# Optimization experiments

Hardware: AMD Instinct MI355X
Metric: run time of the kernel (lower is better)

## Reference

```python
import jax, jax.numpy as jnp
import numpy as np

D_MODEL = 256
N_HEAD = 8
HEAD_DIM = D_MODEL // N_HEAD
N_TOTAL = 24576
B, T = 64, 512


def setup_inputs() -> dict:
    key = jax.random.key(0)
    ks = jax.random.split(key, 12)
    s = 1.0 / np.sqrt(D_MODEL)
    return {
        "x": jax.random.normal(ks[0], (N_TOTAL, D_MODEL), jnp.float32),
        "Wq": jax.random.uniform(ks[1], (D_MODEL, D_MODEL), jnp.float32, -s, s),
        "bq": jax.random.uniform(ks[2], (D_MODEL,), jnp.float32, -s, s),
        "Wk": jax.random.uniform(ks[3], (D_MODEL, D_MODEL), jnp.float32, -s, s),
        "bk": jax.random.uniform(ks[4], (D_MODEL,), jnp.float32, -s, s),
        "Wv": jax.random.uniform(ks[5], (D_MODEL, D_MODEL), jnp.float32, -s, s),
        "bv": jax.random.uniform(ks[6], (D_MODEL,), jnp.float32, -s, s),
        "Wp": jax.random.uniform(ks[7], (D_MODEL, D_MODEL), jnp.float32, -s, s),
        "bp": jax.random.uniform(ks[8], (D_MODEL,), jnp.float32, -s, s),
        "padpack_index": jax.random.randint(ks[9], (B, T), 0, N_TOTAL, jnp.int64 if jax.config.jax_enable_x64 else jnp.int32),
        "padpack_batch": jax.random.randint(ks[10], (B, T), 0, B, jnp.int32),
        "padpack_inverse_index": jax.random.randint(ks[11], (N_TOTAL,), 0, B * T, jnp.int64 if jax.config.jax_enable_x64 else jnp.int32),
    }


def reference(x, Wq, bq, Wk, bk, Wv, bv, Wp, bp, padpack_index, padpack_batch, padpack_inverse_index):
    # gather ragged tokens into packed [B, T, C]
    xp = x[padpack_index]
    # mask: True where packed slots share the same segment id (matches
    # original masked_fill(batch_i == batch_j, -1e9))
    mask = padpack_batch[:, :, None] == padpack_batch[:, None, :]  # [B,T,T]
    # QKV projections (torch Linear: x @ W.T + b), split heads
    def heads(w, b):
        h = xp @ w.T + b
        return h.reshape(B, T, N_HEAD, HEAD_DIM).transpose(0, 2, 1, 3)  # [B,H,T,D]
    q, k, v = heads(Wq, bq), heads(Wk, bk), heads(Wv, bv)
    att = jnp.einsum("bhtd,bhsd->bhts", q, k) * (1.0 / np.sqrt(HEAD_DIM))
    att = jnp.where(mask[:, None], jnp.float32(-1e9), att)
    att = jax.nn.softmax(att, axis=-1)
    y = jnp.einsum("bhts,bhsd->bhtd", att, v)  # [B,H,T,D]
    y = y.transpose(0, 2, 1, 3).reshape(B, T, D_MODEL)
    y = y @ Wp.T + bp
    # scatter back to ragged layout
    return y.reshape(B * T, D_MODEL)[padpack_inverse_index]
```

## Files before the change

### kernel.cpp

```cpp
#include <hip/hip_runtime.h>


typedef __attribute__((ext_vector_type(8))) short short8;
typedef __attribute__((ext_vector_type(4))) float f32x4;

#define N_TOTAL 24576
#define B_ 64
#define T_ 512
#define M_TOK 32768
#define DM 256
#define NH 8
#define HD 32

#define QSCALE 0.25503463f

__device__ __forceinline__ unsigned short f2bf(float f) {
  unsigned int u = __float_as_uint(f);
  u += 0x7fffu + ((u >> 16) & 1u);
  return (unsigned short)(u >> 16);
}

__device__ __forceinline__ void gl_lds16(const void* g, void* l) {
  __builtin_amdgcn_global_load_lds(
      (const __attribute__((address_space(1))) unsigned int*)g,
      (__attribute__((address_space(3))) unsigned int*)l, 16, 0, 0);
}

__global__ __launch_bounds__(256) void pack_kernel(
    const float* __restrict__ x, const float* __restrict__ Wq,
    const float* __restrict__ Wk, const float* __restrict__ Wv,
    const float* __restrict__ Wp, const float* __restrict__ bq,
    const float* __restrict__ bk, const float* __restrict__ bv,
    const int* __restrict__ idx,
    short* __restrict__ XP, short* __restrict__ WCAT, short* __restrict__ WPb,
    float* __restrict__ BCAT) {
  int gid = blockIdx.x * 256 + threadIdx.x;
  if (gid < 768)
    BCAT[gid] = (gid < 256) ? bq[gid] : (gid < 512 ? bk[gid - 256] : bv[gid - 512]);
  const float* src;
  short* dst;
  if (gid < 1048576) {
    int row = gid >> 5, seg = gid & 31;
    src = x + (size_t)idx[row] * DM + seg * 8;
    dst = XP + (size_t)gid * 8;
  } else if (gid < 1073152) {
    int u = gid - 1048576;
    int f = u >> 5, seg = u & 31;
    const float* W = (f < 256) ? Wq : ((f < 512) ? Wk : Wv);
    src = W + (size_t)(f & 255) * DM + seg * 8;
    dst = WCAT + (size_t)u * 8;
  } else {
    int u = gid - 1073152;
    src = Wp + (size_t)u * 8;
    dst = WPb + (size_t)u * 8;
  }
  const float4* s4 = (const float4*)src;
  float4 a = s4[0], b = s4[1];
  short8 o;
  o[0] = (short)f2bf(a.x); o[1] = (short)f2bf(a.y);
  o[2] = (short)f2bf(a.z); o[3] = (short)f2bf(a.w);
  o[4] = (short)f2bf(b.x); o[5] = (short)f2bf(b.y);
  o[6] = (short)f2bf(b.z); o[7] = (short)f2bf(b.w);
  *(short8*)dst = o;
}

__global__ __launch_bounds__(256) void qkv_gemm(
    const short* __restrict__ XP, const short* __restrict__ WCAT,
    const float* __restrict__ BCAT,
    unsigned short* __restrict__ Qb, unsigned short* __restrict__ Kb,
    unsigned short* __restrict__ Vt) {
  __shared__ __align__(16) char smem[3 * 16384];
  int tid = threadIdx.x;
  int lane = tid & 63, w = tid >> 6;
  int i = lane & 15, q = lane >> 4;
  int m0 = blockIdx.x * 128, n0 = blockIdx.y * 128;
  int wm = (w & 1) * 64, wn = (w >> 1) * 64;
  int csa = q ^ ((i >> 1) & 3);

  f32x4 zf = {0.f, 0.f, 0.f, 0.f};
  f32x4 acc[4][4];
#pragma unroll
  for (int mt = 0; mt < 4; mt++)
#pragma unroll
    for (int nt = 0; nt < 4; nt++) acc[mt][nt] = zf;

  auto stage = [&](int k, int s) {
#pragma unroll
    for (int p = 0; p < 2; p++) {
      int U = p * 256 + tid;
      int row = U >> 2, c = U & 3;
      int cs = c ^ ((row >> 1) & 3);
      gl_lds16(XP + (size_t)(m0 + row) * DM + k * 32 + cs * 8,
               smem + s * 16384 + U * 16);
      gl_lds16(WCAT + (size_t)(n0 + row) * DM + k * 32 + cs * 8,
               smem + s * 16384 + 8192 + U * 16);
    }
  };

  stage(0, 0);
  stage(1, 1);
#pragma unroll
  for (int k = 0; k < 8; k++) {
    if (k == 7)
      asm volatile("s_waitcnt vmcnt(0) lgkmcnt(0)\ns_barrier" ::: "memory");
    else
      asm volatile("s_waitcnt vmcnt(4) lgkmcnt(0)\ns_barrier" ::: "memory");
    const short* Asb = (const short*)(smem + (k % 3) * 16384);
    const short* Bsb = Asb + 8192 / 2;
    short8 a[4], bfr[4];
#pragma unroll
    for (int mt = 0; mt < 4; mt++)
      a[mt] = *(const short8*)&Asb[(wm + mt * 16 + i) * 32 + csa * 8];
#pragma unroll
    for (int nt = 0; nt < 4; nt++)
      bfr[nt] = *(const short8*)&Bsb[(wn + nt * 16 + i) * 32 + csa * 8];
    if (k < 6) stage(k + 2, (k + 2) % 3);
#pragma unroll
    for (int mt = 0; mt < 4; mt++)
#pragma unroll
      for (int nt = 0; nt < 4; nt++)
        acc[mt][nt] = __builtin_amdgcn_mfma_f32_16x16x32_bf16(a[mt], bfr[nt], acc[mt][nt], 0, 0, 0);
  }

#pragma unroll
  for (int nt = 0; nt < 4; nt++) {
    int f = n0 + wn + nt * 16 + i;
    float bias = BCAT[f];
    int which = f >> 8;
    int fw = f & 255;
    int hh = fw >> 5, dd = fw & 31;
#pragma unroll
    for (int mt = 0; mt < 4; mt++) {
#pragma unroll
      for (int r = 0; r < 4; r++) {
        int token = m0 + wm + mt * 16 + q * 4 + r;
        int bb = token >> 9, tt = token & 511;
        int bh = bb * NH + hh;
        float val = acc[mt][nt][r] + bias;
        if (which == 0)
          Qb[((size_t)bh * T_ + tt) * HD + dd] = f2bf(val * QSCALE);
        else if (which == 1)
          Kb[((size_t)bh * T_ + tt) * HD + dd] = f2bf(val);
        else
          Vt[((size_t)bh * HD + dd) * T_ + tt] = f2bf(val);
      }
    }
  }
}

__global__ __launch_bounds__(256) void attn_kernel(
    const short* __restrict__ Qb, const short* __restrict__ Kb,
    const short* __restrict__ Vt, const int* __restrict__ batch,
    unsigned short* __restrict__ Y) {
  __shared__ __align__(16) short pscr[4][64 * 40];
  __shared__ int sbat[T_];
  int tid = threadIdx.x, w = tid >> 6, lane = tid & 63;
  int i = lane & 15, q = lane >> 4;
  int bx = blockIdx.x;
  int half = bx >> 9, bh = bx & 511;
  int b = bh >> 3, h = bh & 7;
  int t0 = half * 256 + w * 64;

  *(int2*)&sbat[tid * 2] = *(const int2*)&batch[b * T_ + tid * 2];
  __syncthreads();

  const short* Kbase = Kb + (size_t)bh * T_ * HD;
  const short* Vbase = Vt + (size_t)bh * HD * T_;
  short* pw = &pscr[w][0];

  short8 qf[4];
  unsigned int btpk[4];
#pragma unroll
  for (int mt = 0; mt < 4; mt++)
    qf[mt] = *(const short8*)&Qb[((size_t)bh * T_ + t0 + mt * 16 + i) * HD + q * 8];
#pragma unroll
  for (int mt = 0; mt < 4; mt++) {
    int4 t4 = *(int4*)&sbat[t0 + mt * 16 + q * 4];
    btpk[mt] = (unsigned)t4.x | ((unsigned)t4.y << 8) | ((unsigned)t4.z << 16) |
               ((unsigned)t4.w << 24);
  }

  unsigned short ob = (i == 0) ? (unsigned short)0x3F80 : (unsigned short)0;
  short8 ones = {(short)ob, (short)ob, (short)ob, (short)ob,
                 (short)ob, (short)ob, (short)ob, (short)ob};

  f32x4 zf = {0.f, 0.f, 0.f, 0.f};
  f32x4 o[4][2], lacc[4];
#pragma unroll
  for (int mt = 0; mt < 4; mt++) {
    o[mt][0] = zf; o[mt][1] = zf; lacc[mt] = zf;
  }

  for (int s0 = 0; s0 < T_; s0 += 32) {
    short8 k0f = *(const short8*)&Kbase[(s0 + i) * HD + q * 8];
    short8 k1f = *(const short8*)&Kbase[(s0 + 16 + i) * HD + q * 8];
    short8 v0f = *(const short8*)&Vbase[(size_t)i * T_ + s0 + q * 8];
    short8 v1f = *(const short8*)&Vbase[(size_t)(16 + i) * T_ + s0 + q * 8];
    int bs0 = sbat[s0 + i];
    int bs1 = sbat[s0 + 16 + i];
#pragma unroll
    for (int mt = 0; mt < 4; mt++) {
      f32x4 st0 = __builtin_amdgcn_mfma_f32_16x16x32_bf16(qf[mt], k0f, zf, 0, 0, 0);
      f32x4 st1 = __builtin_amdgcn_mfma_f32_16x16x32_bf16(qf[mt], k1f, zf, 0, 0, 0);
#pragma unroll
      for (int r = 0; r < 4; r++) {
        int btv = (int)((btpk[mt] >> (8 * r)) & 0xffu);
        float e0 = __builtin_amdgcn_exp2f(st0[r]);
        float e1 = __builtin_amdgcn_exp2f(st1[r]);
        unsigned short p0 =
            (btv == bs0) ? (unsigned short)0 : (unsigned short)(__float_as_uint(e0) >> 16);
        unsigned short p1 =
            (btv == bs1) ? (unsigned short)0 : (unsigned short)(__float_as_uint(e1) >> 16);
        pw[(mt * 16 + q * 4 + r) * 40 + i] = (short)p0;
        pw[(mt * 16 + q * 4 + r) * 40 + 16 + i] = (short)p1;
      }
    }
#pragma unroll
    for (int mt = 0; mt < 4; mt++) {
      short8 pa = *(short8*)&pw[(mt * 16 + i) * 40 + q * 8];
      o[mt][0] = __builtin_amdgcn_mfma_f32_16x16x32_bf16(pa, v0f, o[mt][0], 0, 0, 0);
      o[mt][1] = __builtin_amdgcn_mfma_f32_16x16x32_bf16(pa, v1f, o[mt][1], 0, 0, 0);
      lacc[mt] = __builtin_amdgcn_mfma_f32_16x16x32_bf16(pa, ones, lacc[mt], 0, 0, 0);
    }
  }

#pragma unroll
  for (int mt = 0; mt < 4; mt++) {
#pragma unroll
    for (int r = 0; r < 4; r++) {
      float lv = __shfl(lacc[mt][r], lane & 48, 64);
      float inv = __builtin_amdgcn_rcpf(lv);
      size_t yb = ((size_t)b * T_ + t0 + mt * 16 + q * 4 + r) * DM + h * HD;
      Y[yb + i] = f2bf(o[mt][0][r] * inv);
      Y[yb + 16 + i] = f2bf(o[mt][1][r] * inv);
    }
  }
}

__global__ __launch_bounds__(256) void out_gemm(
    const short* __restrict__ Y, const short* __restrict__ WPb,
    const float* __restrict__ bp, const int* __restrict__ inv,
    float* __restrict__ out) {
  __shared__ __align__(16) char smem[3 * 16384];
  int tid = threadIdx.x;
  int lane = tid & 63, w = tid >> 6;
  int i = lane & 15, q = lane >> 4;
  int m0 = blockIdx.x * 128, n0 = blockIdx.y * 128;
  int wm = (w & 1) * 64, wn = (w >> 1) * 64;
  int csa = q ^ ((i >> 1) & 3);

  int iv0 = inv[m0 + (tid >> 2)];
  int iv1 = inv[m0 + 64 + (tid >> 2)];

  f32x4 zf = {0.f, 0.f, 0.f, 0.f};
  f32x4 acc[4][4];
#pragma unroll
  for (int mt = 0; mt < 4; mt++)
#pragma unroll
    for (int nt = 0; nt < 4; nt++) acc[mt][nt] = zf;

  auto stage = [&](int k, int s) {
#pragma unroll
    for (int p = 0; p < 2; p++) {
      int U = p * 256 + tid;
      int row = U >> 2, c = U & 3;
      int cs = c ^ ((row >> 1) & 3);
      int iv = p ? iv1 : iv0;
      gl_lds16(Y + (size_t)iv * DM + k * 32 + cs * 8, smem + s * 16384 + U * 16);
      gl_lds16(WPb + (size_t)(n0 + row) * DM + k * 32 + cs * 8,
               smem + s * 16384 + 8192 + U * 16);
    }
  };

  stage(0, 0);
  stage(1, 1);
#pragma unroll
  for (int k = 0; k < 8; k++) {
    if (k == 7)
      asm volatile("s_waitcnt vmcnt(0) lgkmcnt(0)\ns_barrier" ::: "memory");
    else
      asm volatile("s_waitcnt vmcnt(4) lgkmcnt(0)\ns_barrier" ::: "memory");
    const short* Asb = (const short*)(smem + (k % 3) * 16384);
    const short* Bsb = Asb + 8192 / 2;
    short8 a[4], bfr[4];
#pragma unroll
    for (int mt = 0; mt < 4; mt++)
      a[mt] = *(const short8*)&Asb[(wm + mt * 16 + i) * 32 + csa * 8];
#pragma unroll
    for (int nt = 0; nt < 4; nt++)
      bfr[nt] = *(const short8*)&Bsb[(wn + nt * 16 + i) * 32 + csa * 8];
    if (k < 6) stage(k + 2, (k + 2) % 3);
#pragma unroll
    for (int mt = 0; mt < 4; mt++)
#pragma unroll
      for (int nt = 0; nt < 4; nt++)
        acc[mt][nt] = __builtin_amdgcn_mfma_f32_16x16x32_bf16(a[mt], bfr[nt], acc[mt][nt], 0, 0, 0);
  }

#pragma unroll
  for (int nt = 0; nt < 4; nt++) {
    int f = n0 + wn + nt * 16 + i;
    float bias = bp[f];
#pragma unroll
    for (int mt = 0; mt < 4; mt++) {
#pragma unroll
      for (int r = 0; r < 4; r++) {
        int row = m0 + wm + mt * 16 + q * 4 + r;
        out[(size_t)row * DM + f] = acc[mt][nt][r] + bias;
      }
    }
  }
}

extern "C" void kernel_launch(void* const* d_in, const int* in_sizes, int n_in,
                              void* d_out, int out_size, void* d_ws, size_t ws_size,
                              hipStream_t stream) {
  const float* x = (const float*)d_in[0];
  const float* Wq = (const float*)d_in[1];
  const float* bq = (const float*)d_in[2];
  const float* Wk = (const float*)d_in[3];
  const float* bk = (const float*)d_in[4];
  const float* Wv = (const float*)d_in[5];
  const float* bv = (const float*)d_in[6];
  const float* Wp = (const float*)d_in[7];
  const float* bp = (const float*)d_in[8];
  const int* idx = (const int*)d_in[9];
  const int* batch = (const int*)d_in[10];
  const int* inv = (const int*)d_in[11];
  float* out = (float*)d_out;

  char* ws = (char*)d_ws;
  short* XP = (short*)(ws + 0);
  short* WCAT = (short*)(ws + 16777216);
  short* WPb = (short*)(ws + 17170432);
  float* BCAT = (float*)(ws + 17301504);
  unsigned short* Qb = (unsigned short*)(ws + 17304576);
  unsigned short* Kb = (unsigned short*)(ws + 34081792);
  unsigned short* Vt = (unsigned short*)(ws + 50859008);
  unsigned short* Yb = (unsigned short*)(ws + 67636224);

  pack_kernel<<<4224, 256, 0, stream>>>(x, Wq, Wk, Wv, Wp, bq, bk, bv, idx,
                                        XP, WCAT, WPb, BCAT);
  qkv_gemm<<<dim3(256, 6), 256, 0, stream>>>(XP, WCAT, BCAT, Qb, Kb, Vt);
  attn_kernel<<<1024, 256, 0, stream>>>((const short*)Qb, (const short*)Kb,
                                        (const short*)Vt, batch, Yb);
  out_gemm<<<dim3(192, 2), 256, 0, stream>>>((const short*)Yb, WPb, bp, inv, out);
}
```

Baseline: 191.9 us.

## Keep GEMM B tiles in registers with per-wave A slabs; pack attention P stores

In qkv_gemm and out_gemm, each wave now preloads its 32-column slice of the weight matrix into registers for the whole K range. Each wave also streams its own 64 rows of A into a private LDS slab, which removes the block-wide barriers and the LDS traffic for B. The N tile is halved and the grid doubled, so each block is smaller. The cost is that activation rows are reloaded more often from global memory and duplicated across waves in LDS. In the attention kernel, keys are interleaved per lane so two probabilities can be packed with a byte permute into one 32-bit LDS store, and the segment mask is applied before the exp.

```diff
diff --git a/kernel.cpp b/kernel.cpp
--- a/kernel.cpp
+++ b/kernel.cpp
@@ -7,7 +7,6 @@
 #define N_TOTAL 24576
 #define B_ 64
 #define T_ 512
-#define M_TOK 32768
 #define DM 256
 #define NH 8
 #define HD 32
@@ -69,61 +68,63 @@
     const float* __restrict__ BCAT,
     unsigned short* __restrict__ Qb, unsigned short* __restrict__ Kb,
     unsigned short* __restrict__ Vt) {
-  __shared__ __align__(16) char smem[3 * 16384];
+  __shared__ __align__(16) char smem[4 * 3 * 4096];
   int tid = threadIdx.x;
   int lane = tid & 63, w = tid >> 6;
   int i = lane & 15, q = lane >> 4;
-  int m0 = blockIdx.x * 128, n0 = blockIdx.y * 128;
-  int wm = (w & 1) * 64, wn = (w >> 1) * 64;
+  int m0 = blockIdx.x * 128, n0 = blockIdx.y * 64;
+  int wm = (w & 1) * 64, wn = (w >> 1) * 32;
   int csa = q ^ ((i >> 1) & 3);
+  char* slab0 = smem + w * 12288;
+
+  short8 breg[2][8];
+#pragma unroll
+  for (int nt = 0; nt < 2; nt++)
+#pragma unroll
+    for (int ks = 0; ks < 8; ks++)
+      breg[nt][ks] =
+          *(const short8*)&WCAT[(size_t)(n0 + wn + nt * 16 + i) * DM + ks * 32 + q * 8];
+
+  int srow = lane >> 2;
+  auto stage = [&](int k, int s) {
+    char* sb = slab0 + s * 4096;
+#pragma unroll
+    for (int j = 0; j < 4; j++) {
+      int lr = j * 16 + srow;
+      int c = (lane & 3) ^ ((lr >> 1) & 3);
+      gl_lds16(XP + (size_t)(m0 + wm + lr) * DM + k * 32 + c * 8,
+               sb + j * 1024 + lane * 16);
+    }
+  };
 
   f32x4 zf = {0.f, 0.f, 0.f, 0.f};
-  f32x4 acc[4][4];
-#pragma unroll
-  for (int mt = 0; mt < 4; mt++)
-#pragma unroll
-    for (int nt = 0; nt < 4; nt++) acc[mt][nt] = zf;
-
-  auto stage = [&](int k, int s) {
-#pragma unroll
-    for (int p = 0; p < 2; p++) {
-      int U = p * 256 + tid;
-      int row = U >> 2, c = U & 3;
-      int cs = c ^ ((row >> 1) & 3);
-      gl_lds16(XP + (size_t)(m0 + row) * DM + k * 32 + cs * 8,
-               smem + s * 16384 + U * 16);
-      gl_lds16(WCAT + (size_t)(n0 + row) * DM + k * 32 + cs * 8,
-               smem + s * 16384 + 8192 + U * 16);
-    }
-  };
+  f32x4 acc[4][2];
+#pragma unroll
+  for (int mt = 0; mt < 4; mt++) { acc[mt][0] = zf; acc[mt][1] = zf; }
 
   stage(0, 0);
   stage(1, 1);
 #pragma unroll
   for (int k = 0; k < 8; k++) {
     if (k == 7)
-      asm volatile("s_waitcnt vmcnt(0) lgkmcnt(0)\ns_barrier" ::: "memory");
+      asm volatile("s_waitcnt vmcnt(0)" ::: "memory");
     else
-      asm volatile("s_waitcnt vmcnt(4) lgkmcnt(0)\ns_barrier" ::: "memory");
-    const short* Asb = (const short*)(smem + (k % 3) * 16384);
-    const short* Bsb = Asb + 8192 / 2;
-    short8 a[4], bfr[4];
+      asm volatile("s_waitcnt vmcnt(4)" ::: "memory");
+    const short* Asb = (const short*)(slab0 + (k % 3) * 4096);
+    short8 a[4];
 #pragma unroll
     for (int mt = 0; mt < 4; mt++)
-      a[mt] = *(const short8*)&Asb[(wm + mt * 16 + i) * 32 + csa * 8];
-#pragma unroll
-    for (int nt = 0; nt < 4; nt++)
-      bfr[nt] = *(const short8*)&Bsb[(wn + nt * 16 + i) * 32 + csa * 8];
+      a[mt] = *(const short8*)&Asb[(mt * 16 + i) * 32 + csa * 8];
     if (k < 6) stage(k + 2, (k + 2) % 3);
 #pragma unroll
-    for (int mt = 0; mt < 4; mt++)
-#pragma unroll
-      for (int nt = 0; nt < 4; nt++)
-        acc[mt][nt] = __builtin_amdgcn_mfma_f32_16x16x32_bf16(a[mt], bfr[nt], acc[mt][nt], 0, 0, 0);
-  }
-
-#pragma unroll
-  for (int nt = 0; nt < 4; nt++) {
+    for (int mt = 0; mt < 4; mt++) {
+      acc[mt][0] = __builtin_amdgcn_mfma_f32_16x16x32_bf16(a[mt], breg[0][k], acc[mt][0], 0, 0, 0);
+      acc[mt][1] = __builtin_amdgcn_mfma_f32_16x16x32_bf16(a[mt], breg[1][k], acc[mt][1], 0, 0, 0);
+    }
+  }
+
+#pragma unroll
+  for (int nt = 0; nt < 2; nt++) {
     int f = n0 + wn + nt * 16 + i;
     float bias = BCAT[f];
     int which = f >> 8;
@@ -169,15 +170,14 @@
   short* pw = &pscr[w][0];
 
   short8 qf[4];
-  unsigned int btpk[4];
+  int btv[4][4];
 #pragma unroll
   for (int mt = 0; mt < 4; mt++)
     qf[mt] = *(const short8*)&Qb[((size_t)bh * T_ + t0 + mt * 16 + i) * HD + q * 8];
 #pragma unroll
   for (int mt = 0; mt < 4; mt++) {
     int4 t4 = *(int4*)&sbat[t0 + mt * 16 + q * 4];
-    btpk[mt] = (unsigned)t4.x | ((unsigned)t4.y << 8) | ((unsigned)t4.z << 16) |
-               ((unsigned)t4.w << 24);
+    btv[mt][0] = t4.x; btv[mt][1] = t4.y; btv[mt][2] = t4.z; btv[mt][3] = t4.w;
   }
 
   unsigned short ob = (i == 0) ? (unsigned short)0x3F80 : (unsigned short)0;
@@ -192,27 +192,24 @@
   }
 
   for (int s0 = 0; s0 < T_; s0 += 32) {
-    short8 k0f = *(const short8*)&Kbase[(s0 + i) * HD + q * 8];
-    short8 k1f = *(const short8*)&Kbase[(s0 + 16 + i) * HD + q * 8];
+    short8 k0f = *(const short8*)&Kbase[(s0 + 2 * i) * HD + q * 8];
+    short8 k1f = *(const short8*)&Kbase[(s0 + 2 * i + 1) * HD + q * 8];
     short8 v0f = *(const short8*)&Vbase[(size_t)i * T_ + s0 + q * 8];
     short8 v1f = *(const short8*)&Vbase[(size_t)(16 + i) * T_ + s0 + q * 8];
-    int bs0 = sbat[s0 + i];
-    int bs1 = sbat[s0 + 16 + i];
+    int bs0 = sbat[s0 + 2 * i];
+    int bs1 = sbat[s0 + 2 * i + 1];
 #pragma unroll
     for (int mt = 0; mt < 4; mt++) {
       f32x4 st0 = __builtin_amdgcn_mfma_f32_16x16x32_bf16(qf[mt], k0f, zf, 0, 0, 0);
       f32x4 st1 = __builtin_amdgcn_mfma_f32_16x16x32_bf16(qf[mt], k1f, zf, 0, 0, 0);
 #pragma unroll
       for (int r = 0; r < 4; r++) {
-        int btv = (int)((btpk[mt] >> (8 * r)) & 0xffu);
-        float e0 = __builtin_amdgcn_exp2f(st0[r]);
-        float e1 = __builtin_amdgcn_exp2f(st1[r]);
-        unsigned short p0 =
-            (btv == bs0) ? (unsigned short)0 : (unsigned short)(__float_as_uint(e0) >> 16);
-        unsigned short p1 =
-            (btv == bs1) ? (unsigned short)0 : (unsigned short)(__float_as_uint(e1) >> 16);
-        pw[(mt * 16 + q * 4 + r) * 40 + i] = (short)p0;
-        pw[(mt * 16 + q * 4 + r) * 40 + 16 + i] = (short)p1;
+        float m0v = (btv[mt][r] == bs0) ? -1e9f : st0[r];
+        float m1v = (btv[mt][r] == bs1) ? -1e9f : st1[r];
+        unsigned e0 = __float_as_uint(__builtin_amdgcn_exp2f(m0v));
+        unsigned e1 = __float_as_uint(__builtin_amdgcn_exp2f(m1v));
+        unsigned pk = __builtin_amdgcn_perm(e1, e0, 0x07060302u);
+        *(unsigned*)&pw[(mt * 16 + q * 4 + r) * 40 + 2 * i] = pk;
       }
     }
 #pragma unroll
@@ -241,64 +238,66 @@
     const short* __restrict__ Y, const short* __restrict__ WPb,
     const float* __restrict__ bp, const int* __restrict__ inv,
     float* __restrict__ out) {
-  __shared__ __align__(16) char smem[3 * 16384];
+  __shared__ __align__(16) char smem[4 * 3 * 4096];
   int tid = threadIdx.x;
   int lane = tid & 63, w = tid >> 6;
   int i = lane & 15, q = lane >> 4;
-  int m0 = blockIdx.x * 128, n0 = blockIdx.y * 128;
-  int wm = (w & 1) * 64, wn = (w >> 1) * 64;
+  int m0 = blockIdx.x * 128, n0 = blockIdx.y * 64;
+  int wm = (w & 1) * 64, wn = (w >> 1) * 32;
   int csa = q ^ ((i >> 1) & 3);
-
-  int iv0 = inv[m0 + (tid >> 2)];
-  int iv1 = inv[m0 + 64 + (tid >> 2)];
+  char* slab0 = smem + w * 12288;
+
+  short8 breg[2][8];
+#pragma unroll
+  for (int nt = 0; nt < 2; nt++)
+#pragma unroll
+    for (int ks = 0; ks < 8; ks++)
+      breg[nt][ks] =
+          *(const short8*)&WPb[(size_t)(n0 + wn + nt * 16 + i) * DM + ks * 32 + q * 8];
+
+  int srow = lane >> 2;
+  int ivj[4];
+#pragma unroll
+  for (int j = 0; j < 4; j++) ivj[j] = inv[m0 + wm + j * 16 + srow];
+
+  auto stage = [&](int k, int s) {
+    char* sb = slab0 + s * 4096;
+#pragma unroll
+    for (int j = 0; j < 4; j++) {
+      int lr = j * 16 + srow;
+      int c = (lane & 3) ^ ((lr >> 1) & 3);
+      gl_lds16(Y + (size_t)ivj[j] * DM + k * 32 + c * 8, sb + j * 1024 + lane * 16);
+    }
+  };
 
   f32x4 zf = {0.f, 0.f, 0.f, 0.f};
-  f32x4 acc[4][4];
-#pragma unroll
-  for (int mt = 0; mt < 4; mt++)
-#pragma unroll
-    for (int nt = 0; nt < 4; nt++) acc[mt][nt] = zf;
-
-  auto stage = [&](int k, int s) {
-#pragma unroll
-    for (int p = 0; p < 2; p++) {
-      int U = p * 256 + tid;
-      int row = U >> 2, c = U & 3;
-      int cs = c ^ ((row >> 1) & 3);
-      int iv = p ? iv1 : iv0;
-      gl_lds16(Y + (size_t)iv * DM + k * 32 + cs * 8, smem + s * 16384 + U * 16);
-      gl_lds16(WPb + (size_t)(n0 + row) * DM + k * 32 + cs * 8,
-               smem + s * 16384 + 8192 + U * 16);
-    }
-  };
+  f32x4 acc[4][2];
+#pragma unroll
+  for (int mt = 0; mt < 4; mt++) { acc[mt][0] = zf; acc[mt][1] = zf; }
 
   stage(0, 0);
   stage(1, 1);
 #pragma unroll
   for (int k = 0; k < 8; k++) {
     if (k == 7)
-      asm volatile("s_waitcnt vmcnt(0) lgkmcnt(0)\ns_barrier" ::: "memory");
+      asm volatile("s_waitcnt vmcnt(0)" ::: "memory");
     else
-      asm volatile("s_waitcnt vmcnt(4) lgkmcnt(0)\ns_barrier" ::: "memory");
-    const short* Asb = (const short*)(smem + (k % 3) * 16384);
-    const short* Bsb = Asb + 8192 / 2;
-    short8 a[4], bfr[4];
+      asm volatile("s_waitcnt vmcnt(4)" ::: "memory");
+    const short* Asb = (const short*)(slab0 + (k % 3) * 4096);
+    short8 a[4];
 #pragma unroll
     for (int mt = 0; mt < 4; mt++)
-      a[mt] = *(const short8*)&Asb[(wm + mt * 16 + i) * 32 + csa * 8];
-#pragma unroll
-    for (int nt = 0; nt < 4; nt++)
-      bfr[nt] = *(const short8*)&Bsb[(wn + nt * 16 + i) * 32 + csa * 8];
+      a[mt] = *(const short8*)&Asb[(mt * 16 + i) * 32 + csa * 8];
     if (k < 6) stage(k + 2, (k + 2) % 3);
 #pragma unroll
-    for (int mt = 0; mt < 4; mt++)
-#pragma unroll
-      for (int nt = 0; nt < 4; nt++)
-        acc[mt][nt] = __builtin_amdgcn_mfma_f32_16x16x32_bf16(a[mt], bfr[nt], acc[mt][nt], 0, 0, 0);
-  }
-
-#pragma unroll
-  for (int nt = 0; nt < 4; nt++) {
+    for (int mt = 0; mt < 4; mt++) {
+      acc[mt][0] = __builtin_amdgcn_mfma_f32_16x16x32_bf16(a[mt], breg[0][k], acc[mt][0], 0, 0, 0);
+      acc[mt][1] = __builtin_amdgcn_mfma_f32_16x16x32_bf16(a[mt], breg[1][k], acc[mt][1], 0, 0, 0);
+    }
+  }
+
+#pragma unroll
+  for (int nt = 0; nt < 2; nt++) {
     int f = n0 + wn + nt * 16 + i;
     float bias = bp[f];
 #pragma unroll
@@ -341,8 +340,8 @@
 
   pack_kernel<<<4224, 256, 0, stream>>>(x, Wq, Wk, Wv, Wp, bq, bk, bv, idx,
                                         XP, WCAT, WPb, BCAT);
-  qkv_gemm<<<dim3(256, 6), 256, 0, stream>>>(XP, WCAT, BCAT, Qb, Kb, Vt);
+  qkv_gemm<<<dim3(256, 12), 256, 0, stream>>>(XP, WCAT, BCAT, Qb, Kb, Vt);
   attn_kernel<<<1024, 256, 0, stream>>>((const short*)Qb, (const short*)Kb,
                                         (const short*)Vt, batch, Yb);
-  out_gemm<<<dim3(192, 2), 256, 0, stream>>>((const short*)Yb, WPb, bp, inv, out);
-}
+  out_gemm<<<dim3(192, 4), 256, 0, stream>>>((const short*)Yb, WPb, bp, inv, out);
+}
```

Result: slower. 213.2 us (+11.1%).

## Store QKV token-major and transpose V into LDS inside attention

Applied to the files above, without the earlier changes.

The QKV GEMM now writes one token-major [token, 768] bf16 buffer instead of scattering into per-head Q, K and transposed V layouts, which makes its epilogue stores contiguous. The attention kernel reads Q and K straight from that layout, prefetches the next K tile one iteration ahead, and transposes V into padded shared memory once per block. It also folds the mask in before exp2 and packs two bf16 probabilities per LDS store. In exchange it adds strided K loads, an LDS transpose prologue and more shared memory per block, which may lower occupancy. K rows are interleaved (2i, 2i+1) to match the packed P columns.

```diff
diff --git a/kernel.cpp b/kernel.cpp
--- a/kernel.cpp
+++ b/kernel.cpp
@@ -7,12 +7,13 @@
 #define N_TOTAL 24576
 #define B_ 64
 #define T_ 512
-#define M_TOK 32768
 #define DM 256
 #define NH 8
 #define HD 32
+#define F3 768
 
 #define QSCALE 0.25503463f
+#define VSP 514
 
 __device__ __forceinline__ unsigned short f2bf(float f) {
   unsigned int u = __float_as_uint(f);
@@ -66,9 +67,7 @@
 
 __global__ __launch_bounds__(256) void qkv_gemm(
     const short* __restrict__ XP, const short* __restrict__ WCAT,
-    const float* __restrict__ BCAT,
-    unsigned short* __restrict__ Qb, unsigned short* __restrict__ Kb,
-    unsigned short* __restrict__ Vt) {
+    const float* __restrict__ BCAT, unsigned short* __restrict__ QKVp) {
   __shared__ __align__(16) char smem[3 * 16384];
   int tid = threadIdx.x;
   int lane = tid & 63, w = tid >> 6;
@@ -106,7 +105,7 @@
     else
       asm volatile("s_waitcnt vmcnt(4) lgkmcnt(0)\ns_barrier" ::: "memory");
     const short* Asb = (const short*)(smem + (k % 3) * 16384);
-    const short* Bsb = Asb + 8192 / 2;
+    const short* Bsb = Asb + 4096;
     short8 a[4], bfr[4];
 #pragma unroll
     for (int mt = 0; mt < 4; mt++)
@@ -122,36 +121,26 @@
         acc[mt][nt] = __builtin_amdgcn_mfma_f32_16x16x32_bf16(a[mt], bfr[nt], acc[mt][nt], 0, 0, 0);
   }
 
+  float scale = (n0 < 256) ? QSCALE : 1.0f;
 #pragma unroll
   for (int nt = 0; nt < 4; nt++) {
     int f = n0 + wn + nt * 16 + i;
     float bias = BCAT[f];
-    int which = f >> 8;
-    int fw = f & 255;
-    int hh = fw >> 5, dd = fw & 31;
 #pragma unroll
     for (int mt = 0; mt < 4; mt++) {
 #pragma unroll
       for (int r = 0; r < 4; r++) {
         int token = m0 + wm + mt * 16 + q * 4 + r;
-        int bb = token >> 9, tt = token & 511;
-        int bh = bb * NH + hh;
-        float val = acc[mt][nt][r] + bias;
-        if (which == 0)
-          Qb[((size_t)bh * T_ + tt) * HD + dd] = f2bf(val * QSCALE);
-        else if (which == 1)
-          Kb[((size_t)bh * T_ + tt) * HD + dd] = f2bf(val);
-        else
-          Vt[((size_t)bh * HD + dd) * T_ + tt] = f2bf(val);
+        QKVp[(size_t)token * F3 + f] = f2bf((acc[mt][nt][r] + bias) * scale);
       }
     }
   }
 }
 
 __global__ __launch_bounds__(256) void attn_kernel(
-    const short* __restrict__ Qb, const short* __restrict__ Kb,
-    const short* __restrict__ Vt, const int* __restrict__ batch,
+    const unsigned short* __restrict__ QKVp, const int* __restrict__ batch,
     unsigned short* __restrict__ Y) {
+  __shared__ __align__(16) short Vl[HD * VSP];
   __shared__ __align__(16) short pscr[4][64 * 40];
   __shared__ int sbat[T_];
   int tid = threadIdx.x, w = tid >> 6, lane = tid & 63;
@@ -160,24 +149,33 @@
   int half = bx >> 9, bh = bx & 511;
   int b = bh >> 3, h = bh & 7;
   int t0 = half * 256 + w * 64;
+  const unsigned short* Tok = QKVp + (size_t)b * T_ * F3;
 
   *(int2*)&sbat[tid * 2] = *(const int2*)&batch[b * T_ + tid * 2];
+
+  {
+    int seg = tid & 3, sb = tid >> 2;
+#pragma unroll
+    for (int l = 0; l < 8; l++) {
+      int s = sb + l * 64;
+      short8 v = *(const short8*)&Tok[(size_t)s * F3 + 512 + h * HD + seg * 8];
+#pragma unroll
+      for (int j = 0; j < 8; j++) Vl[(seg * 8 + j) * VSP + s] = v[j];
+    }
+  }
   __syncthreads();
 
-  const short* Kbase = Kb + (size_t)bh * T_ * HD;
-  const short* Vbase = Vt + (size_t)bh * HD * T_;
   short* pw = &pscr[w][0];
 
   short8 qf[4];
-  unsigned int btpk[4];
+  int btv[4][4];
 #pragma unroll
   for (int mt = 0; mt < 4; mt++)
-    qf[mt] = *(const short8*)&Qb[((size_t)bh * T_ + t0 + mt * 16 + i) * HD + q * 8];
+    qf[mt] = *(const short8*)&Tok[(size_t)(t0 + mt * 16 + i) * F3 + h * HD + q * 8];
 #pragma unroll
   for (int mt = 0; mt < 4; mt++) {
     int4 t4 = *(int4*)&sbat[t0 + mt * 16 + q * 4];
-    btpk[mt] = (unsigned)t4.x | ((unsigned)t4.y << 8) | ((unsigned)t4.z << 16) |
-               ((unsigned)t4.w << 24);
+    btv[mt][0] = t4.x; btv[mt][1] = t4.y; btv[mt][2] = t4.z; btv[mt][3] = t4.w;
   }
 
   unsigned short ob = (i == 0) ? (unsigned short)0x3F80 : (unsigned short)0;
@@ -191,28 +189,34 @@
     o[mt][0] = zf; o[mt][1] = zf; lacc[mt] = zf;
   }
 
+  const unsigned short* Kcol = Tok + 256 + h * HD + q * 8;
+  short8 k0f = *(const short8*)&Kcol[(size_t)(2 * i) * F3];
+  short8 k1f = *(const short8*)&Kcol[(size_t)(2 * i + 1) * F3];
+  int bs0 = sbat[2 * i], bs1 = sbat[2 * i + 1];
+
   for (int s0 = 0; s0 < T_; s0 += 32) {
-    short8 k0f = *(const short8*)&Kbase[(s0 + i) * HD + q * 8];
-    short8 k1f = *(const short8*)&Kbase[(s0 + 16 + i) * HD + q * 8];
-    short8 v0f = *(const short8*)&Vbase[(size_t)i * T_ + s0 + q * 8];
-    short8 v1f = *(const short8*)&Vbase[(size_t)(16 + i) * T_ + s0 + q * 8];
-    int bs0 = sbat[s0 + i];
-    int bs1 = sbat[s0 + 16 + i];
+    short8 ck0 = k0f, ck1 = k1f;
+    int cb0 = bs0, cb1 = bs1;
+    if (s0 + 32 < T_) {
+      k0f = *(const short8*)&Kcol[(size_t)(s0 + 32 + 2 * i) * F3];
+      k1f = *(const short8*)&Kcol[(size_t)(s0 + 32 + 2 * i + 1) * F3];
+      bs0 = sbat[s0 + 32 + 2 * i];
+      bs1 = sbat[s0 + 32 + 2 * i + 1];
+    }
+    short8 v0f = *(const short8*)&Vl[i * VSP + s0 + q * 8];
+    short8 v1f = *(const short8*)&Vl[(16 + i) * VSP + s0 + q * 8];
 #pragma unroll
     for (int mt = 0; mt < 4; mt++) {
-      f32x4 st0 = __builtin_amdgcn_mfma_f32_16x16x32_bf16(qf[mt], k0f, zf, 0, 0, 0);
-      f32x4 st1 = __builtin_amdgcn_mfma_f32_16x16x32_bf16(qf[mt], k1f, zf, 0, 0, 0);
+      f32x4 st0 = __builtin_amdgcn_mfma_f32_16x16x32_bf16(qf[mt], ck0, zf, 0, 0, 0);
+      f32x4 st1 = __builtin_amdgcn_mfma_f32_16x16x32_bf16(qf[mt], ck1, zf, 0, 0, 0);
 #pragma unroll
       for (int r = 0; r < 4; r++) {
-        int btv = (int)((btpk[mt] >> (8 * r)) & 0xffu);
-        float e0 = __builtin_amdgcn_exp2f(st0[r]);
-        float e1 = __builtin_amdgcn_exp2f(st1[r]);
-        unsigned short p0 =
-            (btv == bs0) ? (unsigned short)0 : (unsigned short)(__float_as_uint(e0) >> 16);
-        unsigned short p1 =
-            (btv == bs1) ? (unsigned short)0 : (unsigned short)(__float_as_uint(e1) >> 16);
-        pw[(mt * 16 + q * 4 + r) * 40 + i] = (short)p0;
-        pw[(mt * 16 + q * 4 + r) * 40 + 16 + i] = (short)p1;
+        float m0v = (btv[mt][r] == cb0) ? -1e9f : st0[r];
+        float m1v = (btv[mt][r] == cb1) ? -1e9f : st1[r];
+        unsigned e0 = __float_as_uint(__builtin_amdgcn_exp2f(m0v));
+        unsigned e1 = __float_as_uint(__builtin_amdgcn_exp2f(m1v));
+        unsigned pk = __builtin_amdgcn_perm(e1, e0, 0x07060302u);
+        *(unsigned*)&pw[(mt * 16 + q * 4 + r) * 40 + 2 * i] = pk;
       }
     }
 #pragma unroll
@@ -281,7 +285,7 @@
     else
       asm volatile("s_waitcnt vmcnt(4) lgkmcnt(0)\ns_barrier" ::: "memory");
     const short* Asb = (const short*)(smem + (k % 3) * 16384);
-    const short* Bsb = Asb + 8192 / 2;
+    const short* Bsb = Asb + 4096;
     short8 a[4], bfr[4];
 #pragma unroll
     for (int mt = 0; mt < 4; mt++)
@@ -334,15 +338,12 @@
   short* WCAT = (short*)(ws + 16777216);
   short* WPb = (short*)(ws + 17170432);
   float* BCAT = (float*)(ws + 17301504);
-  unsigned short* Qb = (unsigned short*)(ws + 17304576);
-  unsigned short* Kb = (unsigned short*)(ws + 34081792);
-  unsigned short* Vt = (unsigned short*)(ws + 50859008);
+  unsigned short* QKVp = (unsigned short*)(ws + 17304576);
   unsigned short* Yb = (unsigned short*)(ws + 67636224);
 
   pack_kernel<<<4224, 256, 0, stream>>>(x, Wq, Wk, Wv, Wp, bq, bk, bv, idx,
                                         XP, WCAT, WPb, BCAT);
-  qkv_gemm<<<dim3(256, 6), 256, 0, stream>>>(XP, WCAT, BCAT, Qb, Kb, Vt);
-  attn_kernel<<<1024, 256, 0, stream>>>((const short*)Qb, (const short*)Kb,
-                                        (const short*)Vt, batch, Yb);
+  qkv_gemm<<<dim3(256, 6), 256, 0, stream>>>(XP, WCAT, BCAT, QKVp);
+  attn_kernel<<<1024, 256, 0, stream>>>(QKVp, batch, Yb);
   out_gemm<<<dim3(192, 2), 256, 0, stream>>>((const short*)Yb, WPb, bp, inv, out);
 }
```

After: 180.1 us. 6.1% less time.
